# Kernel tuning notes

Hardware: AMD Instinct MI355X
Metric: run time of the kernel (lower is better)

The kernel has to match this reference:

```python
import jax, jax.numpy as jnp
import numpy as np

E = 8        # num experts
K = 2        # top-k
H = 1024     # hidden size
F = 3584     # intermediate (ffn) size
B, S = 1, 2048


def setup_inputs() -> dict:
    key = jax.random.key(0)
    ks = jax.random.split(key, 5)
    scale_h = 1.0 / np.sqrt(H)
    scale_f = 1.0 / np.sqrt(F)
    return {
        "hidden_states": jax.random.normal(ks[0], (B, S, H), jnp.float32),
        "gate_w": jax.random.normal(ks[1], (E, H), jnp.float32) * scale_h,  # Linear [out,in]
        "w1": jax.random.normal(ks[2], (E, F, H), jnp.float32) * scale_h,
        "w3": jax.random.normal(ks[3], (E, F, H), jnp.float32) * scale_h,
        "w2": jax.random.normal(ks[4], (E, H, F), jnp.float32) * scale_f,
    }


def reference(hidden_states, gate_w, w1, w3, w2):
    b, s, h = hidden_states.shape
    x = hidden_states.reshape(-1, h)                       # [T,H]
    T = x.shape[0]
    # Router: softmax over experts, top-k, renormalize
    router_logits = x @ gate_w.T                           # [T,E]
    routing_weights = jax.nn.softmax(router_logits.astype(jnp.float32), axis=-1)
    topk_w, topk_idx = jax.lax.top_k(routing_weights, K)   # [T,K]
    topk_w = topk_w / jnp.sum(topk_w, axis=-1, keepdims=True)
    # Per-token, per-expert combine weight (0 for unselected experts) --
    # matches the original mask-and-sum over all experts.
    tok = jnp.arange(T)
    expert_weights = jnp.zeros((T, E), jnp.float32).at[tok[:, None], topk_idx].add(topk_w)  # [T,E]
    # Dense per-expert SiLU-gated MLP over all tokens (as the reference loop does),
    # vectorized across experts.
    g = jnp.einsum("th,efh->etf", x, w1)                   # [E,T,F]
    u = jnp.einsum("th,efh->etf", x, w3)                   # [E,T,F]
    act = jax.nn.silu(g) * u                               # [E,T,F]
    y = jnp.einsum("etf,ehf->eth", act, w2)                # [E,T,H]
    out = jnp.einsum("eth,te->th", y, expert_weights.astype(y.dtype))  # [T,H]
    return out.reshape(b, s, h)
```

## Files before the change

kernel.cpp:

```cpp
#include <hip/hip_runtime.h>
#include <hip/hip_bf16.h>

#define T_TOK 2048
#define HID   1024
#define FF    3584
#define NE    8
#define TOPK  2
#define GRIDY 24

typedef __bf16 bf16x8 __attribute__((ext_vector_type(8)));
typedef float  f32x4  __attribute__((ext_vector_type(4)));
typedef unsigned short u16x8 __attribute__((ext_vector_type(8)));

#define WS_COUNTS   0u
#define WS_OFFSETS  64u
#define WS_TILECNT  128u
#define WS_TLE      256u
#define WS_TLM      512u
#define WS_TOPKI    4096u
#define WS_TOPKW    20480u
#define WS_SLOTPOS  36864u
#define WS_SLOTROW  53248u
#define WS_ROUTETOK 69632u
#define WS_XG       131072u
#define WS_ACT      (WS_XG + 4096u*1024u*2u)
#define WS_Y        (WS_ACT + 4096u*3584u*2u)

static __device__ __forceinline__ unsigned short f2bf(float f) {
    unsigned int u = __builtin_bit_cast(unsigned int, f);
    u += 0x7FFFu + ((u >> 16) & 1u);
    return (unsigned short)(u >> 16);
}
static __device__ __forceinline__ unsigned int pack2(float a, float b) {
    unsigned int ua = __builtin_bit_cast(unsigned int, a) + 0x8000u;
    unsigned int ub = __builtin_bit_cast(unsigned int, b) + 0x8000u;
    return (ua >> 16) | (ub & 0xFFFF0000u);
}

__global__ __launch_bounds__(256) void k_router(
    const float* __restrict__ x, const float* __restrict__ gw,
    int* __restrict__ counts, int* __restrict__ topki,
    float* __restrict__ topkw, int* __restrict__ slotpos)
{
    int t = blockIdx.x * 4 + (threadIdx.x >> 6);
    int l = threadIdx.x & 63;
    const float* xr = x + (size_t)t * HID;
    float acc[NE];
#pragma unroll
    for (int e = 0; e < NE; ++e) acc[e] = 0.f;
#pragma unroll
    for (int i = 0; i < 4; ++i) {
        int h = l * 4 + i * 256;
        float4 xv = *(const float4*)(xr + h);
#pragma unroll
        for (int e = 0; e < NE; ++e) {
            float4 g = *(const float4*)(gw + e * HID + h);
            acc[e] += xv.x * g.x + xv.y * g.y + xv.z * g.z + xv.w * g.w;
        }
    }
#pragma unroll
    for (int e = 0; e < NE; ++e) {
#pragma unroll
        for (int off = 32; off; off >>= 1) acc[e] += __shfl_xor(acc[e], off);
    }
    if (l == 0) {
        float best = -1e30f, second = -1e30f;
        int bi = 0, si = 0;
#pragma unroll
        for (int e = 0; e < NE; ++e) {
            float v = acc[e];
            if (v > best) { second = best; si = bi; best = v; bi = e; }
            else if (v > second) { second = v; si = e; }
        }
        float w0 = 1.f / (1.f + __expf(second - best));
        float w1 = 1.f - w0;
        topki[2 * t] = bi;  topki[2 * t + 1] = si;
        topkw[2 * t] = w0;  topkw[2 * t + 1] = w1;
        slotpos[2 * t]     = atomicAdd(&counts[bi], 1);
        slotpos[2 * t + 1] = atomicAdd(&counts[si], 1);
    }
}

__global__ void k_prefix(const int* __restrict__ counts, int* __restrict__ offsets,
                         int* __restrict__ tle, int* __restrict__ tlm,
                         int* __restrict__ tilecnt) {
    if (threadIdx.x == 0) {
        int o = 0;
#pragma unroll
        for (int e = 0; e < NE; ++e) { offsets[e] = o; o += counts[e]; }
        int n = 0;
        for (int e = 0; e < NE; ++e) {
            int t = (counts[e] + 255) >> 8;
            for (int i = 0; i < t; ++i) { tle[n] = e; tlm[n] = i; ++n; }
        }
        tilecnt[0] = n;
    }
}

__global__ void k_fill(const int* __restrict__ topki, const int* __restrict__ slotpos,
                       const int* __restrict__ offsets, int* __restrict__ routetok,
                       int* __restrict__ slotrow) {
    int j = blockIdx.x * blockDim.x + threadIdx.x;
    if (j >= T_TOK * TOPK) return;
    int e = topki[j];
    int row = offsets[e] + slotpos[j];
    routetok[row] = j >> 1;
    slotrow[j] = row;
}

__global__ void k_gather(const float* __restrict__ x, const int* __restrict__ routetok,
                         unsigned short* __restrict__ xg) {
    int j = blockIdx.x * blockDim.x + threadIdx.x;
    int r = j >> 8;
    int c = (j & 255) * 4;
    int tok = routetok[r];
    float4 v = *(const float4*)(x + (size_t)tok * HID + c);
    ushort4 o;
    o.x = f2bf(v.x); o.y = f2bf(v.y); o.z = f2bf(v.z); o.w = f2bf(v.w);
    *(ushort4*)(xg + (size_t)r * HID + c) = o;
}

__global__ __launch_bounds__(512, 4) void k_gemm1(
    const unsigned short* __restrict__ xg, const float* __restrict__ w1,
    const float* __restrict__ w3, const int* __restrict__ counts,
    const int* __restrict__ offsets, const int* __restrict__ tle,
    const int* __restrict__ tlm, const int* __restrict__ tilecnt,
    unsigned short* __restrict__ act)
{
    int by = blockIdx.y;
    if (by >= tilecnt[0]) return;
    int e = tle[by];
    int rbase = tlm[by] * 256;
    int cnt = counts[e], obase = offsets[e];
    int fbase = blockIdx.x * 64;

    __shared__ __align__(16) unsigned short lA[256 * 72];
    __shared__ __align__(16) unsigned short lB1[64 * 72];
    __shared__ __align__(16) unsigned short lB3[64 * 72];

    int tid = threadIdx.x;
    const int ra0 = tid >> 3, ca = (tid & 7) * 8;
    const int rb0 = tid >> 4, cb = (tid & 15) * 4;
    const unsigned short* pa[4];
#pragma unroll
    for (int i = 0; i < 4; ++i) {
        int r = obase + rbase + ra0 + 64 * i;
        if (r > 4095) r = 4095;
        pa[i] = xg + (size_t)r * HID + ca;
    }
    const float* w1e = w1 + ((size_t)e * FF + fbase) * HID;
    const float* w3e = w3 + ((size_t)e * FF + fbase) * HID;
    const float* pb1[2];
    const float* pb3[2];
#pragma unroll
    for (int i = 0; i < 2; ++i) {
        pb1[i] = w1e + (size_t)(rb0 + 32 * i) * HID + cb;
        pb3[i] = w3e + (size_t)(rb0 + 32 * i) * HID + cb;
    }

    int lane = tid & 63, wv = tid >> 6, wr = wv >> 1, wc = wv & 1;
    int klane = (lane >> 4) * 8;
    f32x4 accg[4][2], accu[4][2];
#pragma unroll
    for (int m = 0; m < 4; ++m)
#pragma unroll
        for (int n = 0; n < 2; ++n) {
            accg[m][n] = (f32x4){0.f, 0.f, 0.f, 0.f};
            accu[m][n] = (f32x4){0.f, 0.f, 0.f, 0.f};
        }

    u16x8 ra[4]; float4 r1[2], r3[2];
#pragma unroll
    for (int i = 0; i < 4; ++i) ra[i] = *(const u16x8*)(pa[i]);
#pragma unroll
    for (int i = 0; i < 2; ++i) { r1[i] = *(const float4*)(pb1[i]); r3[i] = *(const float4*)(pb3[i]); }

    for (int kt = 0; kt < HID / 64; ++kt) {
#pragma unroll
        for (int i = 0; i < 4; ++i)
            *(u16x8*)(lA + (ra0 + 64 * i) * 72 + ca) = ra[i];
#pragma unroll
        for (int i = 0; i < 2; ++i) {
            uint2 p;
            p.x = pack2(r1[i].x, r1[i].y); p.y = pack2(r1[i].z, r1[i].w);
            *(uint2*)(lB1 + (rb0 + 32 * i) * 72 + cb) = p;
            p.x = pack2(r3[i].x, r3[i].y); p.y = pack2(r3[i].z, r3[i].w);
            *(uint2*)(lB3 + (rb0 + 32 * i) * 72 + cb) = p;
        }
        __syncthreads();
        if (kt < HID / 64 - 1) {
            int kof = (kt + 1) * 64;
#pragma unroll
            for (int i = 0; i < 4; ++i) ra[i] = *(const u16x8*)(pa[i] + kof);
#pragma unroll
            for (int i = 0; i < 2; ++i) {
                r1[i] = *(const float4*)(pb1[i] + kof);
                r3[i] = *(const float4*)(pb3[i] + kof);
            }
        }
#pragma unroll
        for (int kk = 0; kk < 64; kk += 32) {
            int kcol = kk + klane;
            bf16x8 a[4], b1[2], b3[2];
#pragma unroll
            for (int m = 0; m < 4; ++m)
                a[m] = *(const bf16x8*)(lA + (wr * 64 + m * 16 + (lane & 15)) * 72 + kcol);
#pragma unroll
            for (int n = 0; n < 2; ++n) {
                b1[n] = *(const bf16x8*)(lB1 + (wc * 32 + n * 16 + (lane & 15)) * 72 + kcol);
                b3[n] = *(const bf16x8*)(lB3 + (wc * 32 + n * 16 + (lane & 15)) * 72 + kcol);
            }
#pragma unroll
            for (int m = 0; m < 4; ++m)
#pragma unroll
                for (int n = 0; n < 2; ++n) {
                    accg[m][n] = __builtin_amdgcn_mfma_f32_16x16x32_bf16(a[m], b1[n], accg[m][n], 0, 0, 0);
                    accu[m][n] = __builtin_amdgcn_mfma_f32_16x16x32_bf16(a[m], b3[n], accu[m][n], 0, 0, 0);
                }
        }
        __syncthreads();
    }

#pragma unroll
    for (int m = 0; m < 4; ++m)
#pragma unroll
        for (int n = 0; n < 2; ++n)
#pragma unroll
            for (int r = 0; r < 4; ++r) {
                int lr = wr * 64 + m * 16 + (lane >> 4) * 4 + r;
                if (rbase + lr < cnt) {
                    float g = accg[m][n][r], u = accu[m][n][r];
                    float s = g / (1.f + __expf(-g));
                    int col = fbase + wc * 32 + n * 16 + (lane & 15);
                    act[(size_t)(obase + rbase + lr) * FF + col] = f2bf(s * u);
                }
            }
}

__global__ __launch_bounds__(512, 4) void k_gemm2(
    const unsigned short* __restrict__ act, const float* __restrict__ w2,
    const int* __restrict__ counts, const int* __restrict__ offsets,
    const int* __restrict__ tle, const int* __restrict__ tlm,
    const int* __restrict__ tilecnt, float* __restrict__ y)
{
    int by = blockIdx.y;
    if (by >= tilecnt[0]) return;
    int e = tle[by];
    int rbase = tlm[by] * 256;
    int cnt = counts[e], obase = offsets[e];
    int hbase = blockIdx.x * 64;
    int z = blockIdx.z;
    const int kb0 = z * (FF / 2);
    const int KS = FF / 2 / 64;

    __shared__ __align__(16) unsigned short lA[256 * 72];
    __shared__ __align__(16) unsigned short lB[64 * 72];

    int tid = threadIdx.x;
    const int ra0 = tid >> 3, ca = (tid & 7) * 8;
    const int rb0 = tid >> 4, cb = (tid & 15) * 4;
    const unsigned short* pa[4];
#pragma unroll
    for (int i = 0; i < 4; ++i) {
        int r = obase + rbase + ra0 + 64 * i;
        if (r > 4095) r = 4095;
        pa[i] = act + (size_t)r * FF + kb0 + ca;
    }
    const float* w2e = w2 + ((size_t)e * HID + hbase) * FF;
    const float* pb[2];
#pragma unroll
    for (int i = 0; i < 2; ++i)
        pb[i] = w2e + (size_t)(rb0 + 32 * i) * FF + kb0 + cb;

    int lane = tid & 63, wv = tid >> 6, wr = wv >> 1, wc = wv & 1;
    int klane = (lane >> 4) * 8;
    f32x4 acc[4][2];
#pragma unroll
    for (int m = 0; m < 4; ++m)
#pragma unroll
        for (int n = 0; n < 2; ++n) acc[m][n] = (f32x4){0.f, 0.f, 0.f, 0.f};

    u16x8 ra[4]; float4 rw[2];
#pragma unroll
    for (int i = 0; i < 4; ++i) ra[i] = *(const u16x8*)(pa[i]);
#pragma unroll
    for (int i = 0; i < 2; ++i) rw[i] = *(const float4*)(pb[i]);

    for (int kt = 0; kt < KS; ++kt) {
#pragma unroll
        for (int i = 0; i < 4; ++i)
            *(u16x8*)(lA + (ra0 + 64 * i) * 72 + ca) = ra[i];
#pragma unroll
        for (int i = 0; i < 2; ++i) {
            uint2 p;
            p.x = pack2(rw[i].x, rw[i].y); p.y = pack2(rw[i].z, rw[i].w);
            *(uint2*)(lB + (rb0 + 32 * i) * 72 + cb) = p;
        }
        __syncthreads();
        if (kt < KS - 1) {
            int kof = (kt + 1) * 64;
#pragma unroll
            for (int i = 0; i < 4; ++i) ra[i] = *(const u16x8*)(pa[i] + kof);
#pragma unroll
            for (int i = 0; i < 2; ++i) rw[i] = *(const float4*)(pb[i] + kof);
        }
#pragma unroll
        for (int kk = 0; kk < 64; kk += 32) {
            int kcol = kk + klane;
            bf16x8 a[4], b[2];
#pragma unroll
            for (int m = 0; m < 4; ++m)
                a[m] = *(const bf16x8*)(lA + (wr * 64 + m * 16 + (lane & 15)) * 72 + kcol);
#pragma unroll
            for (int n = 0; n < 2; ++n)
                b[n] = *(const bf16x8*)(lB + (wc * 32 + n * 16 + (lane & 15)) * 72 + kcol);
#pragma unroll
            for (int m = 0; m < 4; ++m)
#pragma unroll
                for (int n = 0; n < 2; ++n)
                    acc[m][n] = __builtin_amdgcn_mfma_f32_16x16x32_bf16(a[m], b[n], acc[m][n], 0, 0, 0);
        }
        __syncthreads();
    }

    float* yz = y + (size_t)z * (T_TOK * TOPK * HID);
#pragma unroll
    for (int m = 0; m < 4; ++m)
#pragma unroll
        for (int n = 0; n < 2; ++n)
#pragma unroll
            for (int r = 0; r < 4; ++r) {
                int lr = wr * 64 + m * 16 + (lane >> 4) * 4 + r;
                if (rbase + lr < cnt) {
                    int col = hbase + wc * 32 + n * 16 + (lane & 15);
                    yz[(size_t)(obase + rbase + lr) * HID + col] = acc[m][n][r];
                }
            }
}

__global__ void k_combine(const float* __restrict__ y, const int* __restrict__ slotrow,
                          const float* __restrict__ topkw, float* __restrict__ out) {
    int j = blockIdx.x * blockDim.x + threadIdx.x;
    int t = j >> 8, c = j & 255;
    int r0 = slotrow[2 * t], r1 = slotrow[2 * t + 1];
    float w0 = topkw[2 * t], w1 = topkw[2 * t + 1];
    const float4* y0 = (const float4*)y;
    const float4* y1 = (const float4*)(y + (size_t)T_TOK * TOPK * HID);
    float4 a0 = y0[(size_t)r0 * 256 + c], a1 = y1[(size_t)r0 * 256 + c];
    float4 b0 = y0[(size_t)r1 * 256 + c], b1 = y1[(size_t)r1 * 256 + c];
    float4 o;
    o.x = w0 * (a0.x + a1.x) + w1 * (b0.x + b1.x);
    o.y = w0 * (a0.y + a1.y) + w1 * (b0.y + b1.y);
    o.z = w0 * (a0.z + a1.z) + w1 * (b0.z + b1.z);
    o.w = w0 * (a0.w + a1.w) + w1 * (b0.w + b1.w);
    ((float4*)out)[j] = o;
}

extern "C" void kernel_launch(void* const* d_in, const int* in_sizes, int n_in,
                              void* d_out, int out_size, void* d_ws, size_t ws_size,
                              hipStream_t stream) {
    const float* x  = (const float*)d_in[0];
    const float* gw = (const float*)d_in[1];
    const float* w1 = (const float*)d_in[2];
    const float* w3 = (const float*)d_in[3];
    const float* w2 = (const float*)d_in[4];
    float* out = (float*)d_out;

    char* ws = (char*)d_ws;
    int*   counts   = (int*)(ws + WS_COUNTS);
    int*   offsets  = (int*)(ws + WS_OFFSETS);
    int*   tilecnt  = (int*)(ws + WS_TILECNT);
    int*   tle      = (int*)(ws + WS_TLE);
    int*   tlm      = (int*)(ws + WS_TLM);
    int*   topki    = (int*)(ws + WS_TOPKI);
    float* topkw    = (float*)(ws + WS_TOPKW);
    int*   slotpos  = (int*)(ws + WS_SLOTPOS);
    int*   slotrow  = (int*)(ws + WS_SLOTROW);
    int*   routetok = (int*)(ws + WS_ROUTETOK);
    unsigned short* xg   = (unsigned short*)(ws + WS_XG);
    unsigned short* actb = (unsigned short*)(ws + WS_ACT);
    float* yb = (float*)(ws + WS_Y);

    hipMemsetAsync(counts, 0, 64, stream);
    k_router<<<T_TOK / 4, 256, 0, stream>>>(x, gw, counts, topki, topkw, slotpos);
    k_prefix<<<1, 64, 0, stream>>>(counts, offsets, tle, tlm, tilecnt);
    k_fill<<<16, 256, 0, stream>>>(topki, slotpos, offsets, routetok, slotrow);
    k_gather<<<4096, 256, 0, stream>>>(x, routetok, xg);
    k_gemm1<<<dim3(FF / 64, GRIDY, 1), 512, 0, stream>>>(xg, w1, w3, counts, offsets, tle, tlm, tilecnt, actb);
    k_gemm2<<<dim3(HID / 64, GRIDY, 2), 512, 0, stream>>>(actb, w2, counts, offsets, tle, tlm, tilecnt, yb);
    k_combine<<<2048, 256, 0, stream>>>(yb, slotrow, topkw, out);
}
```

Baseline: 292.3 us.

## Async global-to-LDS double buffering with XOR swizzle and adaptive split-K

Both expert GEMMs now load activation tiles straight into double-buffered LDS with global_load_lds, in place of staging them through registers. An XOR swizzle is baked into the xg and act layouts to avoid LDS bank conflicts, and the padded rows are dropped. Blocks shrink to 256 threads, each wave covering a larger tile: 128 rows, and 128 columns for gemm2. gemm2 split-K becomes 1 to 3 ways depending on workspace size, with combine summing the partials; the bigger accumulators add register pressure and fewer waves per CU.

```diff
diff --git a/kernel.cpp b/kernel.cpp
--- a/kernel.cpp
+++ b/kernel.cpp
@@ -10,7 +10,6 @@
 
 typedef __bf16 bf16x8 __attribute__((ext_vector_type(8)));
 typedef float  f32x4  __attribute__((ext_vector_type(4)));
-typedef unsigned short u16x8 __attribute__((ext_vector_type(8)));
 
 #define WS_COUNTS   0u
 #define WS_OFFSETS  64u
@@ -25,6 +24,7 @@
 #define WS_XG       131072u
 #define WS_ACT      (WS_XG + 4096u*1024u*2u)
 #define WS_Y        (WS_ACT + 4096u*3584u*2u)
+#define Y_STRIDE    (4096u*1024u)
 
 static __device__ __forceinline__ unsigned short f2bf(float f) {
     unsigned int u = __builtin_bit_cast(unsigned int, f);
@@ -35,6 +35,10 @@
     unsigned int ua = __builtin_bit_cast(unsigned int, a) + 0x8000u;
     unsigned int ub = __builtin_bit_cast(unsigned int, b) + 0x8000u;
     return (ua >> 16) | (ub & 0xFFFF0000u);
+}
+static __device__ __forceinline__ void gl_lds16(const void* g, void* l) {
+    __builtin_amdgcn_global_load_lds((const __attribute__((address_space(1))) unsigned int*)g,
+                                     (__attribute__((address_space(3))) unsigned int*)l, 16, 0, 0);
 }
 
 __global__ __launch_bounds__(256) void k_router(
@@ -117,10 +121,11 @@
     float4 v = *(const float4*)(x + (size_t)tok * HID + c);
     ushort4 o;
     o.x = f2bf(v.x); o.y = f2bf(v.y); o.z = f2bf(v.z); o.w = f2bf(v.w);
-    *(ushort4*)(xg + (size_t)r * HID + c) = o;
-}
-
-__global__ __launch_bounds__(512, 4) void k_gemm1(
+    int sc = c ^ ((r & 7) << 3);
+    *(ushort4*)(xg + (size_t)r * HID + sc) = o;
+}
+
+__global__ __launch_bounds__(256, 2) void k_gemm1(
     const unsigned short* __restrict__ xg, const float* __restrict__ w1,
     const float* __restrict__ w3, const int* __restrict__ counts,
     const int* __restrict__ offsets, const int* __restrict__ tle,
@@ -134,225 +139,271 @@
     int cnt = counts[e], obase = offsets[e];
     int fbase = blockIdx.x * 64;
 
-    __shared__ __align__(16) unsigned short lA[256 * 72];
-    __shared__ __align__(16) unsigned short lB1[64 * 72];
-    __shared__ __align__(16) unsigned short lB3[64 * 72];
+    __shared__ __align__(16) unsigned short lA[2][256 * 64];
+    __shared__ __align__(16) unsigned short lB1[64 * 64];
+    __shared__ __align__(16) unsigned short lB3[64 * 64];
 
     int tid = threadIdx.x;
-    const int ra0 = tid >> 3, ca = (tid & 7) * 8;
-    const int rb0 = tid >> 4, cb = (tid & 15) * 4;
-    const unsigned short* pa[4];
-#pragma unroll
-    for (int i = 0; i < 4; ++i) {
-        int r = obase + rbase + ra0 + 64 * i;
-        if (r > 4095) r = 4095;
-        pa[i] = xg + (size_t)r * HID + ca;
-    }
-    const float* w1e = w1 + ((size_t)e * FF + fbase) * HID;
-    const float* w3e = w3 + ((size_t)e * FF + fbase) * HID;
-    const float* pb1[2];
-    const float* pb3[2];
-#pragma unroll
-    for (int i = 0; i < 2; ++i) {
-        pb1[i] = w1e + (size_t)(rb0 + 32 * i) * HID + cb;
-        pb3[i] = w3e + (size_t)(rb0 + 32 * i) * HID + cb;
-    }
-
-    int lane = tid & 63, wv = tid >> 6, wr = wv >> 1, wc = wv & 1;
+    int lane = tid & 63, wv = tid >> 6;
+    int wr = wv >> 1, wc = wv & 1;
+
+    const unsigned short* asrc[8];
+#pragma unroll
+    for (int j = 0; j < 8; ++j) {
+        int r = rbase + (tid >> 3) + 32 * j;
+        int rg = obase + (r < cnt ? r : (cnt - 1));
+        asrc[j] = xg + (size_t)rg * HID + (tid & 7) * 8;
+    }
+    unsigned short* adst = &lA[0][0] + tid * 8;
+
+    int rb = tid & 63;
+    int swzW = (rb & 7) << 3;
+    const float* pb1 = w1 + ((size_t)e * FF + fbase + rb) * HID + wv * 16;
+    const float* pb3 = w3 + ((size_t)e * FF + fbase + rb) * HID + wv * 16;
+    unsigned short* wb1a = lB1 + rb * 64 + ((wv * 16) ^ swzW);
+    unsigned short* wb1b = lB1 + rb * 64 + ((wv * 16 + 8) ^ swzW);
+    unsigned short* wb3a = lB3 + rb * 64 + ((wv * 16) ^ swzW);
+    unsigned short* wb3b = lB3 + rb * 64 + ((wv * 16 + 8) ^ swzW);
+
+    int swzA = (((obase & 7) + (lane & 7)) & 7) << 3;
+    int swzB = (lane & 7) << 3;
     int klane = (lane >> 4) * 8;
-    f32x4 accg[4][2], accu[4][2];
-#pragma unroll
-    for (int m = 0; m < 4; ++m)
+
+    f32x4 accg[8][2], accu[8][2];
+#pragma unroll
+    for (int m = 0; m < 8; ++m)
 #pragma unroll
         for (int n = 0; n < 2; ++n) {
             accg[m][n] = (f32x4){0.f, 0.f, 0.f, 0.f};
             accu[m][n] = (f32x4){0.f, 0.f, 0.f, 0.f};
         }
 
-    u16x8 ra[4]; float4 r1[2], r3[2];
-#pragma unroll
-    for (int i = 0; i < 4; ++i) ra[i] = *(const u16x8*)(pa[i]);
-#pragma unroll
-    for (int i = 0; i < 2; ++i) { r1[i] = *(const float4*)(pb1[i]); r3[i] = *(const float4*)(pb3[i]); }
+#pragma unroll
+    for (int j = 0; j < 8; ++j) gl_lds16(asrc[j], adst + 32 * j * 64);
+    float4 r1[4], r3[4];
+#pragma unroll
+    for (int j = 0; j < 4; ++j) {
+        r1[j] = *(const float4*)(pb1 + 4 * j);
+        r3[j] = *(const float4*)(pb3 + 4 * j);
+    }
 
     for (int kt = 0; kt < HID / 64; ++kt) {
-#pragma unroll
-        for (int i = 0; i < 4; ++i)
-            *(u16x8*)(lA + (ra0 + 64 * i) * 72 + ca) = ra[i];
-#pragma unroll
-        for (int i = 0; i < 2; ++i) {
-            uint2 p;
-            p.x = pack2(r1[i].x, r1[i].y); p.y = pack2(r1[i].z, r1[i].w);
-            *(uint2*)(lB1 + (rb0 + 32 * i) * 72 + cb) = p;
-            p.x = pack2(r3[i].x, r3[i].y); p.y = pack2(r3[i].z, r3[i].w);
-            *(uint2*)(lB3 + (rb0 + 32 * i) * 72 + cb) = p;
-        }
-        __syncthreads();
+        int cur = kt & 1;
+        if (kt < HID / 64 - 1) {
+            unsigned short* nd = &lA[cur ^ 1][0] + tid * 8;
+#pragma unroll
+            for (int j = 0; j < 8; ++j) gl_lds16(asrc[j] + (kt + 1) * 64, nd + 32 * j * 64);
+        }
+        {
+            uint4 q;
+            q.x = pack2(r1[0].x, r1[0].y); q.y = pack2(r1[0].z, r1[0].w);
+            q.z = pack2(r1[1].x, r1[1].y); q.w = pack2(r1[1].z, r1[1].w);
+            *(uint4*)wb1a = q;
+            q.x = pack2(r1[2].x, r1[2].y); q.y = pack2(r1[2].z, r1[2].w);
+            q.z = pack2(r1[3].x, r1[3].y); q.w = pack2(r1[3].z, r1[3].w);
+            *(uint4*)wb1b = q;
+            q.x = pack2(r3[0].x, r3[0].y); q.y = pack2(r3[0].z, r3[0].w);
+            q.z = pack2(r3[1].x, r3[1].y); q.w = pack2(r3[1].z, r3[1].w);
+            *(uint4*)wb3a = q;
+            q.x = pack2(r3[2].x, r3[2].y); q.y = pack2(r3[2].z, r3[2].w);
+            q.z = pack2(r3[3].x, r3[3].y); q.w = pack2(r3[3].z, r3[3].w);
+            *(uint4*)wb3b = q;
+        }
         if (kt < HID / 64 - 1) {
             int kof = (kt + 1) * 64;
 #pragma unroll
-            for (int i = 0; i < 4; ++i) ra[i] = *(const u16x8*)(pa[i] + kof);
-#pragma unroll
-            for (int i = 0; i < 2; ++i) {
-                r1[i] = *(const float4*)(pb1[i] + kof);
-                r3[i] = *(const float4*)(pb3[i] + kof);
-            }
-        }
-#pragma unroll
-        for (int kk = 0; kk < 64; kk += 32) {
-            int kcol = kk + klane;
-            bf16x8 a[4], b1[2], b3[2];
-#pragma unroll
-            for (int m = 0; m < 4; ++m)
-                a[m] = *(const bf16x8*)(lA + (wr * 64 + m * 16 + (lane & 15)) * 72 + kcol);
+            for (int j = 0; j < 4; ++j) {
+                r1[j] = *(const float4*)(pb1 + kof + 4 * j);
+                r3[j] = *(const float4*)(pb3 + kof + 4 * j);
+            }
+        }
+        asm volatile("s_waitcnt lgkmcnt(0)" ::: "memory");
+        __builtin_amdgcn_s_barrier();
+        __builtin_amdgcn_sched_barrier(0);
+        const unsigned short* A = &lA[cur][0];
+#pragma unroll
+        for (int kk = 0; kk < 2; ++kk) {
+            int kc = kk * 32 + klane;
+            int kA = kc ^ swzA, kB = kc ^ swzB;
+            bf16x8 b1f[2], b3f[2];
 #pragma unroll
             for (int n = 0; n < 2; ++n) {
-                b1[n] = *(const bf16x8*)(lB1 + (wc * 32 + n * 16 + (lane & 15)) * 72 + kcol);
-                b3[n] = *(const bf16x8*)(lB3 + (wc * 32 + n * 16 + (lane & 15)) * 72 + kcol);
-            }
-#pragma unroll
-            for (int m = 0; m < 4; ++m)
+                b1f[n] = *(const bf16x8*)(lB1 + (wc * 32 + n * 16 + (lane & 15)) * 64 + kB);
+                b3f[n] = *(const bf16x8*)(lB3 + (wc * 32 + n * 16 + (lane & 15)) * 64 + kB);
+            }
+#pragma unroll
+            for (int m = 0; m < 8; ++m) {
+                bf16x8 a = *(const bf16x8*)(A + (wr * 128 + m * 16 + (lane & 15)) * 64 + kA);
 #pragma unroll
                 for (int n = 0; n < 2; ++n) {
-                    accg[m][n] = __builtin_amdgcn_mfma_f32_16x16x32_bf16(a[m], b1[n], accg[m][n], 0, 0, 0);
-                    accu[m][n] = __builtin_amdgcn_mfma_f32_16x16x32_bf16(a[m], b3[n], accu[m][n], 0, 0, 0);
+                    accg[m][n] = __builtin_amdgcn_mfma_f32_16x16x32_bf16(a, b1f[n], accg[m][n], 0, 0, 0);
+                    accu[m][n] = __builtin_amdgcn_mfma_f32_16x16x32_bf16(a, b3f[n], accu[m][n], 0, 0, 0);
                 }
-        }
-        __syncthreads();
-    }
-
-#pragma unroll
-    for (int m = 0; m < 4; ++m)
+            }
+        }
+        __builtin_amdgcn_sched_barrier(0);
+        asm volatile("s_waitcnt lgkmcnt(0)" ::: "memory");
+        __builtin_amdgcn_s_barrier();
+    }
+
+#pragma unroll
+    for (int m = 0; m < 8; ++m)
 #pragma unroll
         for (int n = 0; n < 2; ++n)
 #pragma unroll
             for (int r = 0; r < 4; ++r) {
-                int lr = wr * 64 + m * 16 + (lane >> 4) * 4 + r;
+                int lr = wr * 128 + m * 16 + (lane >> 4) * 4 + r;
                 if (rbase + lr < cnt) {
                     float g = accg[m][n][r], u = accu[m][n][r];
                     float s = g / (1.f + __expf(-g));
+                    int row = obase + rbase + lr;
                     int col = fbase + wc * 32 + n * 16 + (lane & 15);
-                    act[(size_t)(obase + rbase + lr) * FF + col] = f2bf(s * u);
+                    int scol = col ^ ((row & 7) << 3);
+                    act[(size_t)row * FF + scol] = f2bf(s * u);
                 }
             }
 }
 
-__global__ __launch_bounds__(512, 4) void k_gemm2(
+__global__ __launch_bounds__(256, 2) void k_gemm2(
     const unsigned short* __restrict__ act, const float* __restrict__ w2,
     const int* __restrict__ counts, const int* __restrict__ offsets,
     const int* __restrict__ tle, const int* __restrict__ tlm,
-    const int* __restrict__ tilecnt, float* __restrict__ y)
+    const int* __restrict__ tilecnt, float* __restrict__ y, int ks)
 {
     int by = blockIdx.y;
     if (by >= tilecnt[0]) return;
     int e = tle[by];
     int rbase = tlm[by] * 256;
     int cnt = counts[e], obase = offsets[e];
-    int hbase = blockIdx.x * 64;
+    int hbase = blockIdx.x * 128;
     int z = blockIdx.z;
-    const int kb0 = z * (FF / 2);
-    const int KS = FF / 2 / 64;
-
-    __shared__ __align__(16) unsigned short lA[256 * 72];
-    __shared__ __align__(16) unsigned short lB[64 * 72];
+    const int KTOT = FF / 64;
+    int per = (KTOT + ks - 1) / ks;
+    int kt0 = z * per;
+    int ktn = min(KTOT, kt0 + per) - kt0;
+
+    __shared__ __align__(16) unsigned short lA[2][256 * 64];
+    __shared__ __align__(16) unsigned short lB[128 * 64];
 
     int tid = threadIdx.x;
-    const int ra0 = tid >> 3, ca = (tid & 7) * 8;
-    const int rb0 = tid >> 4, cb = (tid & 15) * 4;
-    const unsigned short* pa[4];
-#pragma unroll
-    for (int i = 0; i < 4; ++i) {
-        int r = obase + rbase + ra0 + 64 * i;
-        if (r > 4095) r = 4095;
-        pa[i] = act + (size_t)r * FF + kb0 + ca;
-    }
-    const float* w2e = w2 + ((size_t)e * HID + hbase) * FF;
-    const float* pb[2];
-#pragma unroll
-    for (int i = 0; i < 2; ++i)
-        pb[i] = w2e + (size_t)(rb0 + 32 * i) * FF + kb0 + cb;
-
-    int lane = tid & 63, wv = tid >> 6, wr = wv >> 1, wc = wv & 1;
+    int lane = tid & 63, wv = tid >> 6;
+    int wr = wv >> 1, wc = wv & 1;
+
+    const unsigned short* asrc[8];
+#pragma unroll
+    for (int j = 0; j < 8; ++j) {
+        int r = rbase + (tid >> 3) + 32 * j;
+        int rg = obase + (r < cnt ? r : (cnt - 1));
+        asrc[j] = act + (size_t)rg * FF + kt0 * 64 + (tid & 7) * 8;
+    }
+    unsigned short* adst = &lA[0][0] + tid * 8;
+
+    int hr = tid & 127, kh = tid >> 7;
+    int swzW = (hr & 7) << 3;
+    const float* pb = w2 + ((size_t)e * HID + hbase + hr) * FF + kt0 * 64 + kh * 32;
+    unsigned short* wb[4];
+#pragma unroll
+    for (int j = 0; j < 4; ++j)
+        wb[j] = lB + hr * 64 + ((kh * 32 + j * 8) ^ swzW);
+
+    int swzA = (((obase & 7) + (lane & 7)) & 7) << 3;
+    int swzB = (lane & 7) << 3;
     int klane = (lane >> 4) * 8;
-    f32x4 acc[4][2];
-#pragma unroll
-    for (int m = 0; m < 4; ++m)
-#pragma unroll
-        for (int n = 0; n < 2; ++n) acc[m][n] = (f32x4){0.f, 0.f, 0.f, 0.f};
-
-    u16x8 ra[4]; float4 rw[2];
-#pragma unroll
-    for (int i = 0; i < 4; ++i) ra[i] = *(const u16x8*)(pa[i]);
-#pragma unroll
-    for (int i = 0; i < 2; ++i) rw[i] = *(const float4*)(pb[i]);
-
-    for (int kt = 0; kt < KS; ++kt) {
-#pragma unroll
-        for (int i = 0; i < 4; ++i)
-            *(u16x8*)(lA + (ra0 + 64 * i) * 72 + ca) = ra[i];
-#pragma unroll
-        for (int i = 0; i < 2; ++i) {
-            uint2 p;
-            p.x = pack2(rw[i].x, rw[i].y); p.y = pack2(rw[i].z, rw[i].w);
-            *(uint2*)(lB + (rb0 + 32 * i) * 72 + cb) = p;
-        }
-        __syncthreads();
-        if (kt < KS - 1) {
+
+    f32x4 acc[8][4];
+#pragma unroll
+    for (int m = 0; m < 8; ++m)
+#pragma unroll
+        for (int n = 0; n < 4; ++n) acc[m][n] = (f32x4){0.f, 0.f, 0.f, 0.f};
+
+#pragma unroll
+    for (int j = 0; j < 8; ++j) gl_lds16(asrc[j], adst + 32 * j * 64);
+    float4 rw[8];
+#pragma unroll
+    for (int j = 0; j < 8; ++j) rw[j] = *(const float4*)(pb + 4 * j);
+
+    for (int kt = 0; kt < ktn; ++kt) {
+        int cur = kt & 1;
+        if (kt < ktn - 1) {
+            unsigned short* nd = &lA[cur ^ 1][0] + tid * 8;
+#pragma unroll
+            for (int j = 0; j < 8; ++j) gl_lds16(asrc[j] + (kt + 1) * 64, nd + 32 * j * 64);
+        }
+        {
+            uint4 q;
+#pragma unroll
+            for (int j = 0; j < 4; ++j) {
+                q.x = pack2(rw[2 * j].x, rw[2 * j].y);
+                q.y = pack2(rw[2 * j].z, rw[2 * j].w);
+                q.z = pack2(rw[2 * j + 1].x, rw[2 * j + 1].y);
+                q.w = pack2(rw[2 * j + 1].z, rw[2 * j + 1].w);
+                *(uint4*)wb[j] = q;
+            }
+        }
+        if (kt < ktn - 1) {
             int kof = (kt + 1) * 64;
 #pragma unroll
-            for (int i = 0; i < 4; ++i) ra[i] = *(const u16x8*)(pa[i] + kof);
-#pragma unroll
-            for (int i = 0; i < 2; ++i) rw[i] = *(const float4*)(pb[i] + kof);
-        }
-#pragma unroll
-        for (int kk = 0; kk < 64; kk += 32) {
-            int kcol = kk + klane;
-            bf16x8 a[4], b[2];
-#pragma unroll
-            for (int m = 0; m < 4; ++m)
-                a[m] = *(const bf16x8*)(lA + (wr * 64 + m * 16 + (lane & 15)) * 72 + kcol);
-#pragma unroll
-            for (int n = 0; n < 2; ++n)
-                b[n] = *(const bf16x8*)(lB + (wc * 32 + n * 16 + (lane & 15)) * 72 + kcol);
-#pragma unroll
-            for (int m = 0; m < 4; ++m)
-#pragma unroll
-                for (int n = 0; n < 2; ++n)
-                    acc[m][n] = __builtin_amdgcn_mfma_f32_16x16x32_bf16(a[m], b[n], acc[m][n], 0, 0, 0);
-        }
-        __syncthreads();
-    }
-
-    float* yz = y + (size_t)z * (T_TOK * TOPK * HID);
-#pragma unroll
-    for (int m = 0; m < 4; ++m)
-#pragma unroll
-        for (int n = 0; n < 2; ++n)
+            for (int j = 0; j < 8; ++j) rw[j] = *(const float4*)(pb + kof + 4 * j);
+        }
+        asm volatile("s_waitcnt lgkmcnt(0)" ::: "memory");
+        __builtin_amdgcn_s_barrier();
+        __builtin_amdgcn_sched_barrier(0);
+        const unsigned short* A = &lA[cur][0];
+#pragma unroll
+        for (int kk = 0; kk < 2; ++kk) {
+            int kc = kk * 32 + klane;
+            int kA = kc ^ swzA, kB = kc ^ swzB;
+            bf16x8 bf[4];
+#pragma unroll
+            for (int n = 0; n < 4; ++n)
+                bf[n] = *(const bf16x8*)(lB + (wc * 64 + n * 16 + (lane & 15)) * 64 + kB);
+#pragma unroll
+            for (int m = 0; m < 8; ++m) {
+                bf16x8 a = *(const bf16x8*)(A + (wr * 128 + m * 16 + (lane & 15)) * 64 + kA);
+#pragma unroll
+                for (int n = 0; n < 4; ++n)
+                    acc[m][n] = __builtin_amdgcn_mfma_f32_16x16x32_bf16(a, bf[n], acc[m][n], 0, 0, 0);
+            }
+        }
+        __builtin_amdgcn_sched_barrier(0);
+        asm volatile("s_waitcnt lgkmcnt(0)" ::: "memory");
+        __builtin_amdgcn_s_barrier();
+    }
+
+    float* yz = y + (size_t)z * Y_STRIDE;
+#pragma unroll
+    for (int m = 0; m < 8; ++m)
+#pragma unroll
+        for (int n = 0; n < 4; ++n)
 #pragma unroll
             for (int r = 0; r < 4; ++r) {
-                int lr = wr * 64 + m * 16 + (lane >> 4) * 4 + r;
+                int lr = wr * 128 + m * 16 + (lane >> 4) * 4 + r;
                 if (rbase + lr < cnt) {
-                    int col = hbase + wc * 32 + n * 16 + (lane & 15);
+                    int col = hbase + wc * 64 + n * 16 + (lane & 15);
                     yz[(size_t)(obase + rbase + lr) * HID + col] = acc[m][n][r];
                 }
             }
 }
 
 __global__ void k_combine(const float* __restrict__ y, const int* __restrict__ slotrow,
-                          const float* __restrict__ topkw, float* __restrict__ out) {
+                          const float* __restrict__ topkw, float* __restrict__ out, int ks) {
     int j = blockIdx.x * blockDim.x + threadIdx.x;
     int t = j >> 8, c = j & 255;
     int r0 = slotrow[2 * t], r1 = slotrow[2 * t + 1];
     float w0 = topkw[2 * t], w1 = topkw[2 * t + 1];
-    const float4* y0 = (const float4*)y;
-    const float4* y1 = (const float4*)(y + (size_t)T_TOK * TOPK * HID);
-    float4 a0 = y0[(size_t)r0 * 256 + c], a1 = y1[(size_t)r0 * 256 + c];
-    float4 b0 = y0[(size_t)r1 * 256 + c], b1 = y1[(size_t)r1 * 256 + c];
+    float4 a = {0.f, 0.f, 0.f, 0.f}, b = {0.f, 0.f, 0.f, 0.f};
+    for (int z = 0; z < ks; ++z) {
+        const float4* yz = (const float4*)(y + (size_t)z * Y_STRIDE);
+        float4 av = yz[(size_t)r0 * 256 + c];
+        float4 bv = yz[(size_t)r1 * 256 + c];
+        a.x += av.x; a.y += av.y; a.z += av.z; a.w += av.w;
+        b.x += bv.x; b.y += bv.y; b.z += bv.z; b.w += bv.w;
+    }
     float4 o;
-    o.x = w0 * (a0.x + a1.x) + w1 * (b0.x + b1.x);
-    o.y = w0 * (a0.y + a1.y) + w1 * (b0.y + b1.y);
-    o.z = w0 * (a0.z + a1.z) + w1 * (b0.z + b1.z);
-    o.w = w0 * (a0.w + a1.w) + w1 * (b0.w + b1.w);
+    o.x = w0 * a.x + w1 * b.x;
+    o.y = w0 * a.y + w1 * b.y;
+    o.z = w0 * a.z + w1 * b.z;
+    o.w = w0 * a.w + w1 * b.w;
     ((float4*)out)[j] = o;
 }
 
@@ -381,12 +432,17 @@
     unsigned short* actb = (unsigned short*)(ws + WS_ACT);
     float* yb = (float*)(ws + WS_Y);
 
+    size_t ybytes = (size_t)Y_STRIDE * 4;
+    int ks = 1;
+    if (ws_size >= (size_t)WS_Y + 3 * ybytes) ks = 3;
+    else if (ws_size >= (size_t)WS_Y + 2 * ybytes) ks = 2;
+
     hipMemsetAsync(counts, 0, 64, stream);
     k_router<<<T_TOK / 4, 256, 0, stream>>>(x, gw, counts, topki, topkw, slotpos);
     k_prefix<<<1, 64, 0, stream>>>(counts, offsets, tle, tlm, tilecnt);
     k_fill<<<16, 256, 0, stream>>>(topki, slotpos, offsets, routetok, slotrow);
     k_gather<<<4096, 256, 0, stream>>>(x, routetok, xg);
-    k_gemm1<<<dim3(FF / 64, GRIDY, 1), 512, 0, stream>>>(xg, w1, w3, counts, offsets, tle, tlm, tilecnt, actb);
-    k_gemm2<<<dim3(HID / 64, GRIDY, 2), 512, 0, stream>>>(actb, w2, counts, offsets, tle, tlm, tilecnt, yb);
-    k_combine<<<2048, 256, 0, stream>>>(yb, slotrow, topkw, out);
-}
+    k_gemm1<<<dim3(FF / 64, GRIDY, 1), 256, 0, stream>>>(xg, w1, w3, counts, offsets, tle, tlm, tilecnt, actb);
+    k_gemm2<<<dim3(HID / 128, GRIDY, ks), 256, 0, stream>>>(actb, w2, counts, offsets, tle, tlm, tilecnt, yb, ks);
+    k_combine<<<2048, 256, 0, stream>>>(yb, slotrow, topkw, out, ks);
+}
```

Result: slower. 322.3 us (+10.3%).

## Double-buffer weight tiles in LDS and use hardware bf16 pack conversion

Applied to the files above, without the earlier changes.

Both expert GEMM kernels now keep two LDS buffers for the fp32-to-bf16 weight tile. Weight global loads are issued two k-steps ahead, and the next tile is converted into the spare buffer before the barrier, with explicit s_barrier and sched_barrier placement. The manual round-to-bf16 pack is replaced by the v_cvt_pk_bf16_f32 instruction, which also changes rounding from add-0x8000 to round-to-nearest-even. The goal is to hide global load latency behind MFMA work and cut conversion ALU cost, at the price of extra LDS and registers that may reduce occupancy.

```diff
diff --git a/kernel.cpp b/kernel.cpp
--- a/kernel.cpp
+++ b/kernel.cpp
@@ -25,16 +25,17 @@
 #define WS_XG       131072u
 #define WS_ACT      (WS_XG + 4096u*1024u*2u)
 #define WS_Y        (WS_ACT + 4096u*3584u*2u)
+#define Y_STRIDE    (4096u*1024u)
 
 static __device__ __forceinline__ unsigned short f2bf(float f) {
     unsigned int u = __builtin_bit_cast(unsigned int, f);
     u += 0x7FFFu + ((u >> 16) & 1u);
     return (unsigned short)(u >> 16);
 }
-static __device__ __forceinline__ unsigned int pack2(float a, float b) {
-    unsigned int ua = __builtin_bit_cast(unsigned int, a) + 0x8000u;
-    unsigned int ub = __builtin_bit_cast(unsigned int, b) + 0x8000u;
-    return (ua >> 16) | (ub & 0xFFFF0000u);
+static __device__ __forceinline__ unsigned int cvtpk(float lo, float hi) {
+    unsigned int r;
+    asm("v_cvt_pk_bf16_f32 %0, %1, %2" : "=v"(r) : "v"(lo), "v"(hi));
+    return r;
 }
 
 __global__ __launch_bounds__(256) void k_router(
@@ -135,8 +136,8 @@
     int fbase = blockIdx.x * 64;
 
     __shared__ __align__(16) unsigned short lA[256 * 72];
-    __shared__ __align__(16) unsigned short lB1[64 * 72];
-    __shared__ __align__(16) unsigned short lB3[64 * 72];
+    __shared__ __align__(16) unsigned short lB1[2][64 * 72];
+    __shared__ __align__(16) unsigned short lB3[2][64 * 72];
 
     int tid = threadIdx.x;
     const int ra0 = tid >> 3, ca = (tid & 7) * 8;
@@ -169,56 +170,76 @@
             accu[m][n] = (f32x4){0.f, 0.f, 0.f, 0.f};
         }
 
-    u16x8 ra[4]; float4 r1[2], r3[2];
-#pragma unroll
-    for (int i = 0; i < 4; ++i) ra[i] = *(const u16x8*)(pa[i]);
+    const int KS = HID / 64;
+    u16x8 rA[4];
+    float4 r1[2], r3[2];
 #pragma unroll
     for (int i = 0; i < 2; ++i) { r1[i] = *(const float4*)(pb1[i]); r3[i] = *(const float4*)(pb3[i]); }
-
-    for (int kt = 0; kt < HID / 64; ++kt) {
+#pragma unroll
+    for (int i = 0; i < 2; ++i) {
+        uint2 p;
+        p.x = cvtpk(r1[i].x, r1[i].y); p.y = cvtpk(r1[i].z, r1[i].w);
+        *(uint2*)(&lB1[0][0] + (rb0 + 32 * i) * 72 + cb) = p;
+        p.x = cvtpk(r3[i].x, r3[i].y); p.y = cvtpk(r3[i].z, r3[i].w);
+        *(uint2*)(&lB3[0][0] + (rb0 + 32 * i) * 72 + cb) = p;
+    }
+#pragma unroll
+    for (int i = 0; i < 4; ++i) rA[i] = *(const u16x8*)(pa[i]);
+#pragma unroll
+    for (int i = 0; i < 2; ++i) { r1[i] = *(const float4*)(pb1[i] + 64); r3[i] = *(const float4*)(pb3[i] + 64); }
+
+    for (int kt = 0; kt < KS; ++kt) {
+        int cur = kt & 1, nx = cur ^ 1;
+        __builtin_amdgcn_sched_barrier(0);
 #pragma unroll
         for (int i = 0; i < 4; ++i)
-            *(u16x8*)(lA + (ra0 + 64 * i) * 72 + ca) = ra[i];
-#pragma unroll
-        for (int i = 0; i < 2; ++i) {
-            uint2 p;
-            p.x = pack2(r1[i].x, r1[i].y); p.y = pack2(r1[i].z, r1[i].w);
-            *(uint2*)(lB1 + (rb0 + 32 * i) * 72 + cb) = p;
-            p.x = pack2(r3[i].x, r3[i].y); p.y = pack2(r3[i].z, r3[i].w);
-            *(uint2*)(lB3 + (rb0 + 32 * i) * 72 + cb) = p;
-        }
-        __syncthreads();
-        if (kt < HID / 64 - 1) {
-            int kof = (kt + 1) * 64;
-#pragma unroll
-            for (int i = 0; i < 4; ++i) ra[i] = *(const u16x8*)(pa[i] + kof);
+            *(u16x8*)(lA + (ra0 + 64 * i) * 72 + ca) = rA[i];
+        if (kt + 1 < KS) {
 #pragma unroll
             for (int i = 0; i < 2; ++i) {
-                r1[i] = *(const float4*)(pb1[i] + kof);
-                r3[i] = *(const float4*)(pb3[i] + kof);
-            }
-        }
-#pragma unroll
-        for (int kk = 0; kk < 64; kk += 32) {
-            int kcol = kk + klane;
-            bf16x8 a[4], b1[2], b3[2];
+                uint2 p;
+                p.x = cvtpk(r1[i].x, r1[i].y); p.y = cvtpk(r1[i].z, r1[i].w);
+                *(uint2*)(&lB1[nx][0] + (rb0 + 32 * i) * 72 + cb) = p;
+                p.x = cvtpk(r3[i].x, r3[i].y); p.y = cvtpk(r3[i].z, r3[i].w);
+                *(uint2*)(&lB3[nx][0] + (rb0 + 32 * i) * 72 + cb) = p;
+            }
+        }
+        asm volatile("s_waitcnt lgkmcnt(0)" ::: "memory");
+        __builtin_amdgcn_s_barrier();
+        __builtin_amdgcn_sched_barrier(0);
+        if (kt + 1 < KS) {
+#pragma unroll
+            for (int i = 0; i < 4; ++i) rA[i] = *(const u16x8*)(pa[i] + (kt + 1) * 64);
+        }
+        if (kt + 2 < KS) {
+#pragma unroll
+            for (int i = 0; i < 2; ++i) {
+                r1[i] = *(const float4*)(pb1[i] + (kt + 2) * 64);
+                r3[i] = *(const float4*)(pb3[i] + (kt + 2) * 64);
+            }
+        }
+#pragma unroll
+        for (int kk = 0; kk < 2; ++kk) {
+            int kcol = kk * 32 + klane;
+            bf16x8 a[4], b1f[2], b3f[2];
 #pragma unroll
             for (int m = 0; m < 4; ++m)
                 a[m] = *(const bf16x8*)(lA + (wr * 64 + m * 16 + (lane & 15)) * 72 + kcol);
 #pragma unroll
             for (int n = 0; n < 2; ++n) {
-                b1[n] = *(const bf16x8*)(lB1 + (wc * 32 + n * 16 + (lane & 15)) * 72 + kcol);
-                b3[n] = *(const bf16x8*)(lB3 + (wc * 32 + n * 16 + (lane & 15)) * 72 + kcol);
+                b1f[n] = *(const bf16x8*)(&lB1[cur][0] + (wc * 32 + n * 16 + (lane & 15)) * 72 + kcol);
+                b3f[n] = *(const bf16x8*)(&lB3[cur][0] + (wc * 32 + n * 16 + (lane & 15)) * 72 + kcol);
             }
 #pragma unroll
             for (int m = 0; m < 4; ++m)
 #pragma unroll
                 for (int n = 0; n < 2; ++n) {
-                    accg[m][n] = __builtin_amdgcn_mfma_f32_16x16x32_bf16(a[m], b1[n], accg[m][n], 0, 0, 0);
-                    accu[m][n] = __builtin_amdgcn_mfma_f32_16x16x32_bf16(a[m], b3[n], accu[m][n], 0, 0, 0);
+                    accg[m][n] = __builtin_amdgcn_mfma_f32_16x16x32_bf16(a[m], b1f[n], accg[m][n], 0, 0, 0);
+                    accu[m][n] = __builtin_amdgcn_mfma_f32_16x16x32_bf16(a[m], b3f[n], accu[m][n], 0, 0, 0);
                 }
         }
-        __syncthreads();
+        __builtin_amdgcn_sched_barrier(0);
+        __builtin_amdgcn_s_barrier();
     }
 
 #pragma unroll
@@ -254,7 +275,7 @@
     const int KS = FF / 2 / 64;
 
     __shared__ __align__(16) unsigned short lA[256 * 72];
-    __shared__ __align__(16) unsigned short lB[64 * 72];
+    __shared__ __align__(16) unsigned short lB[2][64 * 72];
 
     int tid = threadIdx.x;
     const int ra0 = tid >> 3, ca = (tid & 7) * 8;
@@ -280,50 +301,67 @@
 #pragma unroll
         for (int n = 0; n < 2; ++n) acc[m][n] = (f32x4){0.f, 0.f, 0.f, 0.f};
 
-    u16x8 ra[4]; float4 rw[2];
-#pragma unroll
-    for (int i = 0; i < 4; ++i) ra[i] = *(const u16x8*)(pa[i]);
+    u16x8 rA[4];
+    float4 rw[2];
 #pragma unroll
     for (int i = 0; i < 2; ++i) rw[i] = *(const float4*)(pb[i]);
+#pragma unroll
+    for (int i = 0; i < 2; ++i) {
+        uint2 p;
+        p.x = cvtpk(rw[i].x, rw[i].y); p.y = cvtpk(rw[i].z, rw[i].w);
+        *(uint2*)(&lB[0][0] + (rb0 + 32 * i) * 72 + cb) = p;
+    }
+#pragma unroll
+    for (int i = 0; i < 4; ++i) rA[i] = *(const u16x8*)(pa[i]);
+#pragma unroll
+    for (int i = 0; i < 2; ++i) rw[i] = *(const float4*)(pb[i] + 64);
 
     for (int kt = 0; kt < KS; ++kt) {
+        int cur = kt & 1, nx = cur ^ 1;
+        __builtin_amdgcn_sched_barrier(0);
 #pragma unroll
         for (int i = 0; i < 4; ++i)
-            *(u16x8*)(lA + (ra0 + 64 * i) * 72 + ca) = ra[i];
-#pragma unroll
-        for (int i = 0; i < 2; ++i) {
-            uint2 p;
-            p.x = pack2(rw[i].x, rw[i].y); p.y = pack2(rw[i].z, rw[i].w);
-            *(uint2*)(lB + (rb0 + 32 * i) * 72 + cb) = p;
-        }
-        __syncthreads();
-        if (kt < KS - 1) {
-            int kof = (kt + 1) * 64;
-#pragma unroll
-            for (int i = 0; i < 4; ++i) ra[i] = *(const u16x8*)(pa[i] + kof);
-#pragma unroll
-            for (int i = 0; i < 2; ++i) rw[i] = *(const float4*)(pb[i] + kof);
-        }
-#pragma unroll
-        for (int kk = 0; kk < 64; kk += 32) {
-            int kcol = kk + klane;
+            *(u16x8*)(lA + (ra0 + 64 * i) * 72 + ca) = rA[i];
+        if (kt + 1 < KS) {
+#pragma unroll
+            for (int i = 0; i < 2; ++i) {
+                uint2 p;
+                p.x = cvtpk(rw[i].x, rw[i].y); p.y = cvtpk(rw[i].z, rw[i].w);
+                *(uint2*)(&lB[nx][0] + (rb0 + 32 * i) * 72 + cb) = p;
+            }
+        }
+        asm volatile("s_waitcnt lgkmcnt(0)" ::: "memory");
+        __builtin_amdgcn_s_barrier();
+        __builtin_amdgcn_sched_barrier(0);
+        if (kt + 1 < KS) {
+#pragma unroll
+            for (int i = 0; i < 4; ++i) rA[i] = *(const u16x8*)(pa[i] + (kt + 1) * 64);
+        }
+        if (kt + 2 < KS) {
+#pragma unroll
+            for (int i = 0; i < 2; ++i) rw[i] = *(const float4*)(pb[i] + (kt + 2) * 64);
+        }
+#pragma unroll
+        for (int kk = 0; kk < 2; ++kk) {
+            int kcol = kk * 32 + klane;
             bf16x8 a[4], b[2];
 #pragma unroll
             for (int m = 0; m < 4; ++m)
                 a[m] = *(const bf16x8*)(lA + (wr * 64 + m * 16 + (lane & 15)) * 72 + kcol);
 #pragma unroll
             for (int n = 0; n < 2; ++n)
-                b[n] = *(const bf16x8*)(lB + (wc * 32 + n * 16 + (lane & 15)) * 72 + kcol);
+                b[n] = *(const bf16x8*)(&lB[cur][0] + (wc * 32 + n * 16 + (lane & 15)) * 72 + kcol);
 #pragma unroll
             for (int m = 0; m < 4; ++m)
 #pragma unroll
                 for (int n = 0; n < 2; ++n)
                     acc[m][n] = __builtin_amdgcn_mfma_f32_16x16x32_bf16(a[m], b[n], acc[m][n], 0, 0, 0);
         }
-        __syncthreads();
-    }
-
-    float* yz = y + (size_t)z * (T_TOK * TOPK * HID);
+        __builtin_amdgcn_sched_barrier(0);
+        __builtin_amdgcn_s_barrier();
+    }
+
+    float* yz = y + (size_t)z * Y_STRIDE;
 #pragma unroll
     for (int m = 0; m < 4; ++m)
 #pragma unroll
@@ -345,7 +383,7 @@
     int r0 = slotrow[2 * t], r1 = slotrow[2 * t + 1];
     float w0 = topkw[2 * t], w1 = topkw[2 * t + 1];
     const float4* y0 = (const float4*)y;
-    const float4* y1 = (const float4*)(y + (size_t)T_TOK * TOPK * HID);
+    const float4* y1 = (const float4*)(y + (size_t)Y_STRIDE);
     float4 a0 = y0[(size_t)r0 * 256 + c], a1 = y1[(size_t)r0 * 256 + c];
     float4 b0 = y0[(size_t)r1 * 256 + c], b1 = y1[(size_t)r1 * 256 + c];
     float4 o;
```

Measured after the change: 292.9 us. Within noise of the previous version (+0.2%).
